# Kernel tuning notes

Hardware: AMD Instinct MI355X
Metric: run time of the kernel (lower is better)

## Reference

```python
import jax, jax.numpy as jnp
import numpy as np

B, V, E = 1024, 50257, 128

def setup_inputs() -> dict:
    key = jax.random.key(0)
    k1, k2, k3, k4 = jax.random.split(key, 4)
    # xs: one-hot focus-word vectors [B, V]
    focus_ids = jax.random.randint(k1, (B,), 0, V)
    xs = jnp.zeros((B, V), dtype=jnp.float32).at[jnp.arange(B), focus_ids].set(1.0)
    metric = jax.random.normal(k2, (E, E), dtype=jnp.float32)
    EMBEDM = jax.random.normal(k3, (V, E), dtype=jnp.float32)
    NEGEMBEDM = jax.random.normal(k4, (V, E), dtype=jnp.float32)
    return {"xs": xs, "metric": metric, "EMBEDM": EMBEDM, "NEGEMBEDM": NEGEMBEDM}

def reference(xs, metric, EMBEDM, NEGEMBEDM):
    # xs @ EMBEDM : one-hot matmul == row gather, but kept as GEMM to match original math
    xsembeds = xs @ EMBEDM                              # [B, E]
    # dots(vs, ws, metric) = (vs @ metric) @ ws.T
    scores = (xsembeds @ metric) @ NEGEMBEDM.T          # [B, V]
    return jax.nn.log_softmax(scores, axis=1)
```

## Files before the change

### kernel.cpp

```cpp
#include <hip/hip_runtime.h>
#include <hip/hip_bf16.h>
#include <math.h>

#define B_ROWS 1024
#define V_COLS 50257
#define E_DIM  128
#define BM     128
#define BN     128
#define NNB    393
#define VPAD   (NNB * BN)
#define N4     (V_COLS * E_DIM / 4)
#define N4P    (VPAD * E_DIM / 4)
#define NCHUNK 32

typedef __attribute__((ext_vector_type(8))) short short8;
typedef __attribute__((ext_vector_type(4))) float floatx4;

static __device__ __forceinline__ unsigned short f2bf(float x) {
    union { float f; unsigned int u; } c; c.f = x;
    unsigned int u = c.u;
    unsigned int r = u + 0x7fffu + ((u >> 16) & 1u);
    return (unsigned short)(r >> 16);
}

static __device__ __forceinline__ void gload16(const void* g, void* l) {
    __builtin_amdgcn_global_load_lds(
        (const __attribute__((address_space(1))) void*)g,
        (__attribute__((address_space(3))) void*)l,
        16, 0, 0);
}

__global__ void find_idx_kernel(const float* __restrict__ xs, int* __restrict__ idx) {
    long i = (long)blockIdx.x * blockDim.x + threadIdx.x;
    const long n4 = (long)B_ROWS * V_COLS / 4;
    if (i >= n4) return;
    floatx4 v = __builtin_nontemporal_load((const floatx4*)xs + i);
    float vals[4] = {v.x, v.y, v.z, v.w};
    #pragma unroll
    for (int c = 0; c < 4; ++c) {
        if (vals[c] != 0.0f) {
            long f = 4 * i + c;
            int b = (int)(f / V_COLS);
            idx[b] = (int)(f - (long)b * V_COLS);
        }
    }
}

__global__ void cvt_bf16_kernel(const float* __restrict__ src, ushort4* __restrict__ dst) {
    int i = blockIdx.x * blockDim.x + threadIdx.x;
    if (i >= N4P) return;
    ushort4 o;
    if (i < N4) {
        floatx4 v = __builtin_nontemporal_load((const floatx4*)src + i);
        o.x = f2bf(v.x); o.y = f2bf(v.y); o.z = f2bf(v.z); o.w = f2bf(v.w);
    } else {
        o.x = 0; o.y = 0; o.z = 0; o.w = 0;
    }
    dst[i] = o;
}

__global__ void compute_t_kernel(const float* __restrict__ EMB, const float* __restrict__ metric,
                                 const int* __restrict__ idx, unsigned short* __restrict__ t) {
    __shared__ float erow[E_DIM];
    int b = blockIdx.x, tid = threadIdx.x;
    int id = idx[b];
    erow[tid] = EMB[(long)id * E_DIM + tid];
    __syncthreads();
    float acc = 0.f;
    #pragma unroll 16
    for (int k = 0; k < E_DIM; ++k) acc += erow[k] * metric[k * E_DIM + tid];
    t[b * E_DIM + tid] = f2bf(acc);
}

template <bool WRITE_OUT>
__global__ __launch_bounds__(512, 2) void gemm_chunk_kernel(const unsigned short* __restrict__ t,
                                                            const unsigned short* __restrict__ neg,
                                                            float2* __restrict__ partials,
                                                            const float* __restrict__ lse,
                                                            float* __restrict__ out) {
    __shared__ __align__(16) uint4 bbuf[2][2048];

    const int lin  = blockIdx.x;
    const int m    = (lin >> 3) & 7;
    const int c    = (lin & 7) | ((lin >> 6) << 3);
    const int t0   = (c * NNB) / NCHUNK;
    const int t1   = ((c + 1) * NNB) / NCHUNK;

    const int tid  = threadIdx.x;
    const int lane = tid & 63, wave = tid >> 6;
    const int l16  = lane & 15, q = lane >> 4;
    const int wm   = wave >> 2, wn = wave & 3;
    const int mbase = m * BM;

    short8 af[4][4];
    #pragma unroll
    for (int mf = 0; mf < 4; ++mf)
        #pragma unroll
        for (int ks = 0; ks < 4; ++ks)
            af[mf][ks] = *(const short8*)&t[(size_t)(mbase + wm * 64 + mf * 16 + l16) * E_DIM + ks * 32 + q * 8];

    float lsev[4][4];
    float mrun[4][4], srun[4][4];
    if (WRITE_OUT) {
        #pragma unroll
        for (int mf = 0; mf < 4; ++mf)
            #pragma unroll
            for (int r = 0; r < 4; ++r)
                lsev[mf][r] = lse[mbase + wm * 64 + mf * 16 + q * 4 + r];
    } else {
        #pragma unroll
        for (int mf = 0; mf < 4; ++mf)
            #pragma unroll
            for (int r = 0; r < 4; ++r) { mrun[mf][r] = -INFINITY; srun[mf][r] = 0.f; }
    }

    const int p0 = wave * 256 + lane;
    auto STAGE = [&](int buf, int tile) {
        const uint4* srcB = (const uint4*)(neg + (size_t)tile * BN * E_DIM);
        #pragma unroll
        for (int i = 0; i < 4; ++i) {
            int p = p0 + i * 64;
            int r = p >> 4, cc = p & 15;
            int s = (r << 4) + (cc ^ (r & 15));
            gload16(srcB + s, &bbuf[buf][wave * 256 + i * 64]);
        }
    };

    STAGE(0, t0);
    __syncthreads();

    for (int tt = t0; tt < t1; ++tt) {
        const int cur = (tt - t0) & 1;
        if (tt + 1 < t1) STAGE(cur ^ 1, tt + 1);

        floatx4 acc[4][2];
        #pragma unroll
        for (int i = 0; i < 4; ++i)
            #pragma unroll
            for (int j = 0; j < 2; ++j) acc[i][j] = (floatx4){0, 0, 0, 0};

        #pragma unroll
        for (int ks = 0; ks < 4; ++ks) {
            short8 bfr[2];
            #pragma unroll
            for (int nf = 0; nf < 2; ++nf) {
                int row = wn * 32 + nf * 16 + l16;
                bfr[nf] = *(const short8*)&bbuf[cur][(row << 4) + ((ks * 4 + q) ^ (row & 15))];
            }
            #pragma unroll
            for (int mf = 0; mf < 4; ++mf)
                #pragma unroll
                for (int nf = 0; nf < 2; ++nf)
                    acc[mf][nf] = __builtin_amdgcn_mfma_f32_16x16x32_bf16(af[mf][ks], bfr[nf], acc[mf][nf], 0, 0, 0);
        }

        const int col0 = tt * BN + wn * 32 + l16;
        const bool v0 = col0 < V_COLS;
        const bool v1 = (col0 + 16) < V_COLS;

        if (!WRITE_OUT) {
            #pragma unroll
            for (int mf = 0; mf < 4; ++mf)
                #pragma unroll
                for (int r = 0; r < 4; ++r) {
                    float a0 = v0 ? acc[mf][0][r] : -INFINITY;
                    float a1 = v1 ? acc[mf][1][r] : -INFINITY;
                    float nm = fmaxf(mrun[mf][r], fmaxf(a0, a1));
                    float s  = srun[mf][r] * __expf(mrun[mf][r] - nm);
                    if (v0) s += __expf(a0 - nm);
                    if (v1) s += __expf(a1 - nm);
                    mrun[mf][r] = nm; srun[mf][r] = s;
                }
        } else {
            #pragma unroll
            for (int mf = 0; mf < 4; ++mf) {
                const size_t rowb = (size_t)(mbase + wm * 64 + mf * 16 + q * 4) * V_COLS;
                #pragma unroll
                for (int r = 0; r < 4; ++r) {
                    if (v0) out[rowb + (size_t)r * V_COLS + col0]      = acc[mf][0][r] - lsev[mf][r];
                    if (v1) out[rowb + (size_t)r * V_COLS + col0 + 16] = acc[mf][1][r] - lsev[mf][r];
                }
            }
        }
        __syncthreads();
    }

    if (!WRITE_OUT) {
        #pragma unroll
        for (int mf = 0; mf < 4; ++mf)
            #pragma unroll
            for (int r = 0; r < 4; ++r) {
                float mm = mrun[mf][r], ss = srun[mf][r];
                #pragma unroll
                for (int d = 1; d < 16; d <<= 1) {
                    float mo = __shfl_xor(mm, d, 16);
                    float so = __shfl_xor(ss, d, 16);
                    float nm = fmaxf(mm, mo);
                    ss = ss * __expf(mm - nm) + so * __expf(mo - nm);
                    mm = nm;
                }
                if (l16 == 0) {
                    int row_local = wm * 64 + mf * 16 + q * 4 + r;
                    partials[(((size_t)mbase + row_local) * NCHUNK + c) * 4 + wn] = make_float2(mm, ss);
                }
            }
    }
}

__global__ __launch_bounds__(128) void merge_lse_kernel(const float2* __restrict__ partials,
                                                        float* __restrict__ lse) {
    int b = blockIdx.x, tid = threadIdx.x;
    float2 p = partials[(size_t)b * 128 + tid];
    float mm = p.x, ss = p.y;
    #pragma unroll
    for (int d = 1; d < 64; d <<= 1) {
        float mo = __shfl_xor(mm, d, 64);
        float so = __shfl_xor(ss, d, 64);
        float nm = fmaxf(mm, mo);
        ss = ss * __expf(mm - nm) + so * __expf(mo - nm);
        mm = nm;
    }
    __shared__ float m2[2], s2[2];
    if ((tid & 63) == 0) { m2[tid >> 6] = mm; s2[tid >> 6] = ss; }
    __syncthreads();
    if (tid == 0) {
        float nm = fmaxf(m2[0], m2[1]);
        float s  = s2[0] * __expf(m2[0] - nm) + s2[1] * __expf(m2[1] - nm);
        lse[b] = nm + __logf(s);
    }
}

extern "C" void kernel_launch(void* const* d_in, const int* in_sizes, int n_in,
                              void* d_out, int out_size, void* d_ws, size_t ws_size,
                              hipStream_t stream) {
    const float* xs     = (const float*)d_in[0];
    const float* metric = (const float*)d_in[1];
    const float* EMB    = (const float*)d_in[2];
    const float* NEG    = (const float*)d_in[3];
    float* out = (float*)d_out;

    char* ws = (char*)d_ws;
    int*            idx      = (int*)ws;
    unsigned short* t        = (unsigned short*)(ws + 4096);
    unsigned short* neg16    = (unsigned short*)(ws + 266240);
    float2*         partials = (float2*)(ws + 13144064);
    float*          lse      = (float*)(ws + 14192640);

    {
        long n4 = (long)B_ROWS * V_COLS / 4;
        int blocks = (int)((n4 + 255) / 256);
        find_idx_kernel<<<blocks, 256, 0, stream>>>(xs, idx);
    }
    cvt_bf16_kernel<<<(N4P + 255) / 256, 256, 0, stream>>>(NEG, (ushort4*)neg16);
    compute_t_kernel<<<B_ROWS, E_DIM, 0, stream>>>(EMB, metric, idx, t);
    gemm_chunk_kernel<false><<<8 * NCHUNK, 512, 0, stream>>>(t, neg16, partials, nullptr, nullptr);
    merge_lse_kernel<<<B_ROWS, 128, 0, stream>>>(partials, lse);
    gemm_chunk_kernel<true><<<8 * NCHUNK, 512, 0, stream>>>(t, neg16, partials, lse, out);
}
```

Before: 438.5 us.

## Merge prep kernels, lazy-rescale online softmax, nontemporal output stores

```diff
diff --git a/kernel.cpp b/kernel.cpp
--- a/kernel.cpp
+++ b/kernel.cpp
@@ -12,6 +12,8 @@
 #define N4     (V_COLS * E_DIM / 4)
 #define N4P    (VPAD * E_DIM / 4)
 #define NCHUNK 32
+#define CVT_BLOCKS ((N4P + 255) / 256)
+#define FI_BLOCKS  ((B_ROWS * V_COLS / 4 + 255) / 256)
 
 typedef __attribute__((ext_vector_type(8))) short short8;
 typedef __attribute__((ext_vector_type(4))) float floatx4;
@@ -30,33 +32,35 @@
         16, 0, 0);
 }
 
-__global__ void find_idx_kernel(const float* __restrict__ xs, int* __restrict__ idx) {
-    long i = (long)blockIdx.x * blockDim.x + threadIdx.x;
-    const long n4 = (long)B_ROWS * V_COLS / 4;
-    if (i >= n4) return;
-    floatx4 v = __builtin_nontemporal_load((const floatx4*)xs + i);
-    float vals[4] = {v.x, v.y, v.z, v.w};
-    #pragma unroll
-    for (int c = 0; c < 4; ++c) {
-        if (vals[c] != 0.0f) {
-            long f = 4 * i + c;
-            int b = (int)(f / V_COLS);
-            idx[b] = (int)(f - (long)b * V_COLS);
-        }
-    }
-}
-
-__global__ void cvt_bf16_kernel(const float* __restrict__ src, ushort4* __restrict__ dst) {
-    int i = blockIdx.x * blockDim.x + threadIdx.x;
-    if (i >= N4P) return;
-    ushort4 o;
-    if (i < N4) {
-        floatx4 v = __builtin_nontemporal_load((const floatx4*)src + i);
-        o.x = f2bf(v.x); o.y = f2bf(v.y); o.z = f2bf(v.z); o.w = f2bf(v.w);
+__global__ void prep_kernel(const float* __restrict__ xs, int* __restrict__ idx,
+                            const float* __restrict__ NEG, ushort4* __restrict__ dst) {
+    const int bid = blockIdx.x;
+    if (bid < CVT_BLOCKS) {
+        int i = bid * 256 + threadIdx.x;
+        if (i >= N4P) return;
+        ushort4 o;
+        if (i < N4) {
+            floatx4 v = __builtin_nontemporal_load((const floatx4*)NEG + i);
+            o.x = f2bf(v.x); o.y = f2bf(v.y); o.z = f2bf(v.z); o.w = f2bf(v.w);
+        } else {
+            o.x = 0; o.y = 0; o.z = 0; o.w = 0;
+        }
+        dst[i] = o;
     } else {
-        o.x = 0; o.y = 0; o.z = 0; o.w = 0;
-    }
-    dst[i] = o;
+        long i = (long)(bid - CVT_BLOCKS) * 256 + threadIdx.x;
+        const long n4 = (long)B_ROWS * V_COLS / 4;
+        if (i >= n4) return;
+        floatx4 v = __builtin_nontemporal_load((const floatx4*)xs + i);
+        float vals[4] = {v.x, v.y, v.z, v.w};
+        #pragma unroll
+        for (int c = 0; c < 4; ++c) {
+            if (vals[c] != 0.0f) {
+                long f = 4 * i + c;
+                int b = (int)(f / V_COLS);
+                idx[b] = (int)(f - (long)b * V_COLS);
+            }
+        }
+    }
 }
 
 __global__ void compute_t_kernel(const float* __restrict__ EMB, const float* __restrict__ metric,
@@ -154,31 +158,63 @@
                     acc[mf][nf] = __builtin_amdgcn_mfma_f32_16x16x32_bf16(af[mf][ks], bfr[nf], acc[mf][nf], 0, 0, 0);
         }
 
-        const int col0 = tt * BN + wn * 32 + l16;
-        const bool v0 = col0 < V_COLS;
-        const bool v1 = (col0 + 16) < V_COLS;
+        const bool tail = ((tt + 1) * BN > V_COLS);
+        const int  col0 = tt * BN + wn * 32 + l16;
 
         if (!WRITE_OUT) {
-            #pragma unroll
-            for (int mf = 0; mf < 4; ++mf)
-                #pragma unroll
-                for (int r = 0; r < 4; ++r) {
-                    float a0 = v0 ? acc[mf][0][r] : -INFINITY;
-                    float a1 = v1 ? acc[mf][1][r] : -INFINITY;
-                    float nm = fmaxf(mrun[mf][r], fmaxf(a0, a1));
-                    float s  = srun[mf][r] * __expf(mrun[mf][r] - nm);
-                    if (v0) s += __expf(a0 - nm);
-                    if (v1) s += __expf(a1 - nm);
-                    mrun[mf][r] = nm; srun[mf][r] = s;
-                }
+            if (!tail) {
+                #pragma unroll
+                for (int mf = 0; mf < 4; ++mf)
+                    #pragma unroll
+                    for (int r = 0; r < 4; ++r) {
+                        float a0 = acc[mf][0][r], a1 = acc[mf][1][r];
+                        float pm = fmaxf(a0, a1);
+                        float m0 = mrun[mf][r];
+                        if (pm > m0 + 8.f) { srun[mf][r] *= __expf(m0 - pm); mrun[mf][r] = pm; m0 = pm; }
+                        srun[mf][r] += __expf(a0 - m0) + __expf(a1 - m0);
+                    }
+            } else {
+                const bool v0 = col0 < V_COLS;
+                const bool v1 = (col0 + 16) < V_COLS;
+                #pragma unroll
+                for (int mf = 0; mf < 4; ++mf)
+                    #pragma unroll
+                    for (int r = 0; r < 4; ++r) {
+                        float a0 = v0 ? acc[mf][0][r] : -INFINITY;
+                        float a1 = v1 ? acc[mf][1][r] : -INFINITY;
+                        float pm = fmaxf(a0, a1);
+                        float m0 = mrun[mf][r];
+                        if (pm > m0 + 8.f) { srun[mf][r] *= __expf(m0 - pm); mrun[mf][r] = pm; m0 = pm; }
+                        if (v0) srun[mf][r] += __expf(a0 - m0);
+                        if (v1) srun[mf][r] += __expf(a1 - m0);
+                    }
+            }
         } else {
-            #pragma unroll
-            for (int mf = 0; mf < 4; ++mf) {
-                const size_t rowb = (size_t)(mbase + wm * 64 + mf * 16 + q * 4) * V_COLS;
-                #pragma unroll
-                for (int r = 0; r < 4; ++r) {
-                    if (v0) out[rowb + (size_t)r * V_COLS + col0]      = acc[mf][0][r] - lsev[mf][r];
-                    if (v1) out[rowb + (size_t)r * V_COLS + col0 + 16] = acc[mf][1][r] - lsev[mf][r];
+            if (!tail) {
+                #pragma unroll
+                for (int mf = 0; mf < 4; ++mf) {
+                    const size_t rowb = (size_t)(mbase + wm * 64 + mf * 16 + q * 4) * V_COLS;
+                    #pragma unroll
+                    for (int r = 0; r < 4; ++r) {
+                        __builtin_nontemporal_store(acc[mf][0][r] - lsev[mf][r],
+                                                    &out[rowb + (size_t)r * V_COLS + col0]);
+                        __builtin_nontemporal_store(acc[mf][1][r] - lsev[mf][r],
+                                                    &out[rowb + (size_t)r * V_COLS + col0 + 16]);
+                    }
+                }
+            } else {
+                const bool v0 = col0 < V_COLS;
+                const bool v1 = (col0 + 16) < V_COLS;
+                #pragma unroll
+                for (int mf = 0; mf < 4; ++mf) {
+                    const size_t rowb = (size_t)(mbase + wm * 64 + mf * 16 + q * 4) * V_COLS;
+                    #pragma unroll
+                    for (int r = 0; r < 4; ++r) {
+                        if (v0) __builtin_nontemporal_store(acc[mf][0][r] - lsev[mf][r],
+                                                            &out[rowb + (size_t)r * V_COLS + col0]);
+                        if (v1) __builtin_nontemporal_store(acc[mf][1][r] - lsev[mf][r],
+                                                            &out[rowb + (size_t)r * V_COLS + col0 + 16]);
+                    }
                 }
             }
         }
@@ -246,12 +282,7 @@
     float2*         partials = (float2*)(ws + 13144064);
     float*          lse      = (float*)(ws + 14192640);
 
-    {
-        long n4 = (long)B_ROWS * V_COLS / 4;
-        int blocks = (int)((n4 + 255) / 256);
-        find_idx_kernel<<<blocks, 256, 0, stream>>>(xs, idx);
-    }
-    cvt_bf16_kernel<<<(N4P + 255) / 256, 256, 0, stream>>>(NEG, (ushort4*)neg16);
+    prep_kernel<<<CVT_BLOCKS + FI_BLOCKS, 256, 0, stream>>>(xs, idx, NEG, (ushort4*)neg16);
     compute_t_kernel<<<B_ROWS, E_DIM, 0, stream>>>(EMB, metric, idx, t);
     gemm_chunk_kernel<false><<<8 * NCHUNK, 512, 0, stream>>>(t, neg16, partials, nullptr, nullptr);
     merge_lse_kernel<<<B_ROWS, 128, 0, stream>>>(partials, lse);
```

New measurement: 517.4 us. 18.0% more time.
